# Optimization experiments

Measured on AMD Instinct MI355X. Metric: run time of the kernel, lower is better.

The kernel has to match this reference:

```python
import jax, jax.numpy as jnp
import numpy as np

D = 512
H = 8
DH = D // H
EPS = 1e-6


def _ln(x, g, b):
    m = x.mean(-1, keepdims=True)
    v = ((x - m) ** 2).mean(-1, keepdims=True)
    return g * (x - m) / jnp.sqrt(v + EPS) + b


def _mha(q_in, kv_in, W, B):
    # W: [4, D, D] = (Wq, Wk, Wv, Wo); B: [4, D]
    q = q_in @ W[0] + B[0]
    k = kv_in @ W[1] + B[1]
    v = kv_in @ W[2] + B[2]

    def split(t):
        b, l, _ = t.shape
        return t.reshape(b, l, H, DH).transpose(0, 2, 1, 3)  # [b,h,l,dh]

    q, k, v = split(q), split(k), split(v)
    s = jnp.einsum('bhqd,bhkd->bhqk', q, k) / np.sqrt(DH).astype(np.float32)
    a = jax.nn.softmax(s, axis=-1)
    o = jnp.einsum('bhqk,bhkd->bhqd', a, v)
    b_, _, l, _ = o.shape
    o = o.transpose(0, 2, 1, 3).reshape(b_, l, D)
    return o @ W[3] + B[3]


def _cross_layer(x, y, attn_w, attn_b, w1, b1, w2, b2, lns):
    # pre-norm residual sublayers (annotated-transformer style), dropout in eval mode
    x = x + _mha(_ln(x, lns[0, 0], lns[0, 1]), y, attn_w, attn_b)
    h = _ln(x, lns[1, 0], lns[1, 1])
    x = x + (jax.nn.relu(h @ w1 + b1) @ w2 + b2)
    return x


def _af(q, k, v, Wq, bq, Wo, bo):
    # AF with proj=True: single-head attention scaled by sqrt(embed_dim)
    q = q @ Wq + bq
    s = jnp.einsum('bqd,bkd->bqk', q, k) / np.sqrt(D).astype(np.float32)
    o = jax.nn.softmax(s, axis=-1) @ v
    return o @ Wo + bo


def _forward(x, text, vis,
             ft_attn_w, ft_attn_b, ft_w1, ft_b1, ft_w2, ft_b2, ft_ln,
             fv_attn_w, fv_attn_b, fv_w1, fv_b1, fv_w2, fv_b2, fv_ln,
             ldm_ln, af_w, af_b):
    # mode='y', proj=True path
    med = _cross_layer(vis, text, ft_attn_w, ft_attn_b, ft_w1, ft_b1, ft_w2, ft_b2, ft_ln)
    med = _cross_layer(med, vis, fv_attn_w, fv_attn_b, fv_w1, fv_b1, fv_w2, fv_b2, fv_ln) + med
    med = _ln(med, ldm_ln[0], ldm_ln[1])
    # FDIntervention: af_1(mediator, feature, feature) then af_2(feature, mediator, v)
    v = _af(med, x, x, af_w[0, 0], af_b[0, 0], af_w[0, 1], af_b[0, 1])
    out = _af(x, med, v, af_w[1, 0], af_b[1, 0], af_w[1, 1], af_b[1, 1])
    return out + x


def setup_inputs() -> dict:
    key = jax.random.key(0)
    ks = jax.random.split(key, 16)
    B, LX, LT, LV = 32, 256, 256, 196
    sc = 0.02

    def ln_pair():
        # [2(sublayers), 2(gamma,beta), D]
        return jnp.stack([jnp.stack([jnp.ones((D,)), jnp.zeros((D,))])] * 2)

    return {
        'x': jax.random.normal(ks[0], (B, LX, D), jnp.float32),
        'text': jax.random.normal(ks[1], (B, LT, D), jnp.float32),
        'vis': jax.random.normal(ks[2], (B, LV, D), jnp.float32),
        'ft_attn_w': jax.random.normal(ks[3], (4, D, D), jnp.float32) * sc,
        'ft_attn_b': jnp.zeros((4, D), jnp.float32),
        'ft_w1': jax.random.normal(ks[4], (D, 4 * D), jnp.float32) * sc,
        'ft_b1': jnp.zeros((4 * D,), jnp.float32),
        'ft_w2': jax.random.normal(ks[5], (4 * D, D), jnp.float32) * sc,
        'ft_b2': jnp.zeros((D,), jnp.float32),
        'ft_ln': ln_pair(),
        'fv_attn_w': jax.random.normal(ks[6], (4, D, D), jnp.float32) * sc,
        'fv_attn_b': jnp.zeros((4, D), jnp.float32),
        'fv_w1': jax.random.normal(ks[7], (D, 4 * D), jnp.float32) * sc,
        'fv_b1': jnp.zeros((4 * D,), jnp.float32),
        'fv_w2': jax.random.normal(ks[8], (4 * D, D), jnp.float32) * sc,
        'fv_b2': jnp.zeros((D,), jnp.float32),
        'fv_ln': ln_pair(),
        'ldm_ln': jnp.stack([jnp.ones((D,)), jnp.zeros((D,))]),
        'af_w': jax.random.normal(ks[9], (2, 2, D, D), jnp.float32) * sc,
        'af_b': jnp.zeros((2, 2, D), jnp.float32),
    }


def reference(x, text, vis,
              ft_attn_w, ft_attn_b, ft_w1, ft_b1, ft_w2, ft_b2, ft_ln,
              fv_attn_w, fv_attn_b, fv_w1, fv_b1, fv_w2, fv_b2, fv_ln,
              ldm_ln, af_w, af_b):
    return _forward(x, text, vis,
                    ft_attn_w, ft_attn_b, ft_w1, ft_b1, ft_w2, ft_b2, ft_ln,
                    fv_attn_w, fv_attn_b, fv_w1, fv_b1, fv_w2, fv_b2, fv_ln,
                    ldm_ln, af_w, af_b)
```

## Files before the change

### kernel.cpp

```cpp
#include <hip/hip_runtime.h>
#include <hip/hip_bf16.h>

typedef __attribute__((ext_vector_type(4))) float f32x4;
typedef __attribute__((ext_vector_type(8))) short s16x8;
typedef __attribute__((ext_vector_type(4))) short s16x4;

__device__ __forceinline__ short f2bf(float f) {
  union { float f; unsigned u; } c; c.f = f;
  unsigned r = c.u + 0x7fffu + ((c.u >> 16) & 1u);
  return (short)(r >> 16);
}
__device__ __forceinline__ float bf2f(short h) {
  union { unsigned u; float f; } c; c.u = ((unsigned)(unsigned short)h) << 16;
  return c.f;
}
__device__ __forceinline__ s16x8 cvt8(const f32x4& lo, const f32x4& hi) {
  s16x8 v;
  v[0] = f2bf(lo[0]); v[1] = f2bf(lo[1]); v[2] = f2bf(lo[2]); v[3] = f2bf(lo[3]);
  v[4] = f2bf(hi[0]); v[5] = f2bf(hi[1]); v[6] = f2bf(hi[2]); v[7] = f2bf(hi[3]);
  return v;
}

__device__ __forceinline__ void gl_lds16(const short* g, char* l) {
  __builtin_amdgcn_global_load_lds(
      (const __attribute__((address_space(1))) unsigned int*)g,
      (__attribute__((address_space(3))) unsigned int*)l, 16, 0, 0);
}

template<int CF32, int BM, int BN, int WRN, int WCN, int RING,
         int SM, int RELU, int NRES, int BIASM, int SWZ>
__global__ __launch_bounds__(WRN * WCN * 64, 2)
void gemm_k(const short* __restrict__ Ap, int hbA, long sAo, long sAi, int lda,
            const short* __restrict__ Bp, int hbB, long sBo, long sBi, int ldb,
            void* __restrict__ Cp, int hbC, long sCo, long sCi, int ldc,
            const float* __restrict__ bias,
            const float* __restrict__ res1,
            const float* __restrict__ res2,
            int M, int N, int K, float alpha, int nvalid)
{
  constexpr int WAVES = WRN * WCN;
  constexpr int T = WAVES * 64;
  constexpr int MI = BM / (WRN * 16), NI = BN / (WCN * 16);
  constexpr int ACH = BM * 8 / T, BCH = BN * 8 / T;
  constexpr int L   = ACH + BCH;
  constexpr int ABYTES = BM * 128;
  constexpr int TBYTES = (BM + BN) * 128;
  constexpr int LSTR = BN + (CF32 ? 4 : 8);
  constexpr int EPIB = BM * LSTR * (CF32 ? 4 : 2);
  constexpr int SMEMB = (RING * TBYTES > EPIB) ? RING * TBYTES : EPIB;
  __shared__ __align__(16) char smem[SMEMB];

  const int tid  = threadIdx.x;
  const int lane = tid & 63;
  const int wid  = tid >> 6;
  const int wr   = wid / WCN, wc = wid % WCN;

  int bx = blockIdx.x, by = blockIdx.y, bz = blockIdx.z;
  if constexpr (SWZ == 1) {
    const int gx = gridDim.x, gy = gridDim.y;
    const int nwg = gx * gy;
    const int o = by * gx + bx;
    const int q = nwg >> 3, r = nwg & 7;
    const int xcd = o & 7, slot = o >> 3;
    const int w = (xcd < r ? xcd * (q + 1) : r * (q + 1) + (xcd - r) * q) + slot;
    bx = w / gy; by = w - bx * gy;
  } else if constexpr (SWZ == 2) {
    const int gx = gridDim.x, gy = gridDim.y, gz = gridDim.z;
    const int nwg = gx * gy * gz;
    const int o = (bz * gy + by) * gx + bx;
    const int q = nwg >> 3, r = nwg & 7;
    const int xcd = o & 7, slot = o >> 3;
    int w = (xcd < r ? xcd * (q + 1) : r * (q + 1) + (xcd - r) * q) + slot;
    bx = w % gx; w /= gx; by = w % gy; bz = w / gy;
  }
  const int m0 = bx * BM, n0 = by * BN;
  const int z  = bz;

  const int zA = z / hbA, zAi = z - zA * hbA;
  const int zB = z / hbB, zBi = z - zB * hbB;
  const int zC = z / hbC, zCi = z - zC * hbC;
  const short* Ab = Ap + (long)zA * sAo + (long)zAi * sAi;
  const short* Bb = Bp + (long)zB * sBo + (long)zBi * sBi;
  char*        Cb = (char*)Cp + ((long)zC * sCo + (long)zCi * sCi) * (CF32 ? 4 : 2);

  int aL[ACH]; long aG[ACH];
#pragma unroll
  for (int j = 0; j < ACH; ++j) {
    int chunk = (j * WAVES + wid) * 64 + lane;
    int row = chunk >> 3;
    int c   = (chunk & 7) ^ (row & 7);
    int gr = m0 + row; if (gr > M - 1) gr = M - 1;
    aL[j] = chunk * 16;
    aG[j] = (long)gr * lda + c * 8;
  }
  int bL[BCH]; long bG[BCH];
#pragma unroll
  for (int j = 0; j < BCH; ++j) {
    int chunk = (j * WAVES + wid) * 64 + lane;
    int row = chunk >> 3;
    int c   = (chunk & 7) ^ (row & 7);
    int gc = n0 + row; if (gc > N - 1) gc = N - 1;
    bL[j] = chunk * 16;
    bG[j] = (long)gc * ldb + c * 8;
  }

  auto stage = [&](int buf, int kt) {
    const short* Akt = Ab + (long)kt * 64;
    char* base = smem + buf * TBYTES;
#pragma unroll
    for (int j = 0; j < ACH; ++j) gl_lds16(Akt + aG[j], base + aL[j]);
    const short* Bkt = Bb + (long)kt * 64;
#pragma unroll
    for (int j = 0; j < BCH; ++j) gl_lds16(Bkt + bG[j], base + ABYTES + bL[j]);
  };

  int ard[2][MI], brd[2][NI];
#pragma unroll
  for (int kk = 0; kk < 2; ++kk) {
    int kgr = kk * 4 + (lane >> 4);
#pragma unroll
    for (int mi = 0; mi < MI; ++mi) {
      int m = wr * (BM / WRN) + mi * 16 + (lane & 15);
      ard[kk][mi] = m * 128 + ((kgr ^ (m & 7)) << 4);
    }
#pragma unroll
    for (int ni = 0; ni < NI; ++ni) {
      int n = wc * (BN / WCN) + ni * 16 + (lane & 15);
      brd[kk][ni] = ABYTES + n * 128 + ((kgr ^ (n & 7)) << 4);
    }
  }

  const int NT = K >> 6;
#pragma unroll
  for (int p = 0; p < RING; ++p) if (p < NT) stage(p, p);

  f32x4 acc[MI][NI];
#pragma unroll
  for (int mi = 0; mi < MI; ++mi)
#pragma unroll
    for (int ni = 0; ni < NI; ++ni) acc[mi][ni] = (f32x4){0.f, 0.f, 0.f, 0.f};

  int bufi = 0;
  for (int t = 0; t < NT; ++t) {
    const int rem = NT - t;
    if constexpr (RING == 3) {
      if (rem >= 3)      asm volatile("s_waitcnt vmcnt(%0)" :: "n"(2 * L) : "memory");
      else if (rem == 2) asm volatile("s_waitcnt vmcnt(%0)" :: "n"(L) : "memory");
      else               asm volatile("s_waitcnt vmcnt(0)" ::: "memory");
    } else if constexpr (RING == 2) {
      if (rem >= 2)      asm volatile("s_waitcnt vmcnt(%0)" :: "n"(L) : "memory");
      else               asm volatile("s_waitcnt vmcnt(0)" ::: "memory");
    } else {
      asm volatile("s_waitcnt vmcnt(0)" ::: "memory");
    }
    asm volatile("s_barrier" ::: "memory");

    const char* base = smem + bufi * TBYTES;
#pragma unroll
    for (int kk = 0; kk < 2; ++kk) {
      s16x8 af[MI];
#pragma unroll
      for (int mi = 0; mi < MI; ++mi) af[mi] = *(const s16x8*)(base + ard[kk][mi]);
#pragma unroll
      for (int ni = 0; ni < NI; ++ni) {
        s16x8 bf = *(const s16x8*)(base + brd[kk][ni]);
#pragma unroll
        for (int mi = 0; mi < MI; ++mi)
          acc[mi][ni] = __builtin_amdgcn_mfma_f32_16x16x32_bf16(af[mi], bf, acc[mi][ni], 0, 0, 0);
      }
    }

    if (t + RING < NT) {
      asm volatile("s_waitcnt lgkmcnt(0)" ::: "memory");
      asm volatile("s_barrier" ::: "memory");
      stage(bufi, t + RING);
    }
    bufi = (bufi + 1 == RING) ? 0 : bufi + 1;
  }

  if constexpr (SM) {
#pragma unroll
    for (int mi = 0; mi < MI; ++mi) {
#pragma unroll
      for (int j = 0; j < 4; ++j) {
        float mx = -3.0e38f;
#pragma unroll
        for (int ni = 0; ni < NI; ++ni) {
          int col = n0 + wc * (BN / WCN) + ni * 16 + (lane & 15);
          float s = acc[mi][ni][j] * alpha;
          acc[mi][ni][j] = (col < nvalid) ? s : -3.0e38f;
          mx = fmaxf(mx, acc[mi][ni][j]);
        }
#pragma unroll
        for (int o = 1; o < 16; o <<= 1) mx = fmaxf(mx, __shfl_xor(mx, o));
        float sum = 0.f;
#pragma unroll
        for (int ni = 0; ni < NI; ++ni) {
          int col = n0 + wc * (BN / WCN) + ni * 16 + (lane & 15);
          float e = (col < nvalid) ? __expf(acc[mi][ni][j] - mx) : 0.f;
          acc[mi][ni][j] = e;
          sum += e;
        }
#pragma unroll
        for (int o = 1; o < 16; o <<= 1) sum += __shfl_xor(sum, o);
        float inv = 1.f / sum;
#pragma unroll
        for (int ni = 0; ni < NI; ++ni) acc[mi][ni][j] *= inv;
      }
    }
  }
  const float aep = SM ? 1.f : alpha;

  asm volatile("s_waitcnt lgkmcnt(0)" ::: "memory");
  __syncthreads();

  {
    float* lf = (float*)smem;
    short* lh = (short*)smem;
#pragma unroll
    for (int mi = 0; mi < MI; ++mi)
#pragma unroll
      for (int ni = 0; ni < NI; ++ni) {
        int c_loc = wc * (BN / WCN) + ni * 16 + (lane & 15);
        float bv = (bias && !BIASM) ? bias[n0 + c_loc] : 0.f;
        int rb = wr * (BM / WRN) + mi * 16 + ((lane >> 4) << 2);
#pragma unroll
        for (int j = 0; j < 4; ++j) {
          float v = acc[mi][ni][j] * aep + bv;
          if constexpr (CF32) lf[(rb + j) * LSTR + c_loc] = v;
          else                lh[(rb + j) * LSTR + c_loc] = f2bf(v);
        }
      }
  }
  __syncthreads();

  constexpr int CPR = BN / 8;
  constexpr int RP  = T / CPR;
  const int rr0 = tid / CPR;
  const int cc  = (tid % CPR) * 8;
  for (int r = rr0; r < BM; r += RP) {
    const int gr = m0 + r;
    if (gr >= M) break;
    f32x4 a, b;
    if constexpr (CF32) {
      a = *(const f32x4*)((const float*)smem + (long)r * LSTR + cc);
      b = *(const f32x4*)((const float*)smem + (long)r * LSTR + cc + 4);
    } else {
      s16x8 h = *(const s16x8*)((const short*)smem + (long)r * LSTR + cc);
#pragma unroll
      for (int j = 0; j < 4; ++j) { a[j] = bf2f(h[j]); b[j] = bf2f(h[j + 4]); }
    }
    if constexpr (BIASM) {
      float bm = bias[gr];
#pragma unroll
      for (int j = 0; j < 4; ++j) { a[j] += bm; b[j] += bm; }
    }
    const long gb = (long)gr * ldc + n0 + cc;
    if constexpr (NRES >= 1) {
      f32x4 r1 = *(const f32x4*)(res1 + gb), r2 = *(const f32x4*)(res1 + gb + 4);
#pragma unroll
      for (int j = 0; j < 4; ++j) { a[j] += r1[j]; b[j] += r2[j]; }
    }
    if constexpr (NRES >= 2) {
      f32x4 r1 = *(const f32x4*)(res2 + gb), r2 = *(const f32x4*)(res2 + gb + 4);
#pragma unroll
      for (int j = 0; j < 4; ++j) { a[j] += r1[j]; b[j] += r2[j]; }
    }
    if constexpr (RELU) {
#pragma unroll
      for (int j = 0; j < 4; ++j) { a[j] = fmaxf(a[j], 0.f); b[j] = fmaxf(b[j], 0.f); }
    }
    if constexpr (CF32) {
      *(f32x4*)((float*)Cb + gb) = a;
      *(f32x4*)((float*)Cb + gb + 4) = b;
    } else {
      *(s16x8*)((short*)Cb + gb) = cvt8(a, b);
    }
  }
}

__global__ __launch_bounds__(256, 2)
void mha_k(const short* __restrict__ Qp, long qStride,
           const short* __restrict__ Kp, long kStride, int ldk, int Lkv,
           const short* __restrict__ VTp, long vtStride,
           short* __restrict__ Op, int Lq, float alpha, int nvalid)
{
  __shared__ __align__(16) char smem[73728];
  char* Qs  = smem;
  char* Ks  = smem + 8192;
  char* VTs = smem + 40960;

  const int tid = threadIdx.x, lane = tid & 63, wid = tid >> 6;

  int bxr = blockIdx.x, bzr = blockIdx.z;
  {
    const int gx = gridDim.x, gz = gridDim.z;
    const int nwg = gx * gz;
    const int o = bzr * gx + bxr;
    const int q = nwg >> 3, r = nwg & 7;
    const int xcd = o & 7, slot = o >> 3;
    int w = (xcd < r ? xcd * (q + 1) : r * (q + 1) + (xcd - r) * q) + slot;
    bxr = w % gx; bzr = w / gx;
  }
  const int z = bzr, b = z >> 3, h = z & 7;
  const int m0 = bxr * 64;

  const short* Qb  = Qp + (long)b * qStride + h * 64;
  const short* Kb  = Kp + (long)b * kStride + h * 64;
  const short* VTb = VTp + (long)z * vtStride;
  short*       Ob  = Op + (long)b * qStride + h * 64;

#pragma unroll
  for (int j = 0; j < 2; ++j) {
    int chunk = (j * 4 + wid) * 64 + lane;
    int row = chunk >> 3, c = (chunk & 7) ^ (row & 7);
    int gr = m0 + row; if (gr > Lq - 1) gr = Lq - 1;
    gl_lds16(Qb + (long)gr * 512 + c * 8, Qs + chunk * 16);
  }
#pragma unroll
  for (int j = 0; j < 8; ++j) {
    int chunk = (j * 4 + wid) * 64 + lane;
    int row = chunk >> 3, c = (chunk & 7) ^ (row & 7);
    int gr = row; if (gr > Lkv - 1) gr = Lkv - 1;
    gl_lds16(Kb + (long)gr * ldk + c * 8, Ks + chunk * 16);
  }
#pragma unroll
  for (int j = 0; j < 8; ++j) {
    int chunk = (j * 4 + wid) * 64 + lane;
    int row = chunk >> 5, cw = (chunk & 31) ^ (row & 15);
    gl_lds16(VTb + (long)row * 256 + cw * 8, VTs + chunk * 16);
  }
  __syncthreads();

  f32x4 acc[16];
#pragma unroll
  for (int ni = 0; ni < 16; ++ni) acc[ni] = (f32x4){0.f, 0.f, 0.f, 0.f};
#pragma unroll
  for (int kk = 0; kk < 2; ++kk) {
    int kgr = kk * 4 + (lane >> 4);
    int m = wid * 16 + (lane & 15);
    s16x8 af = *(const s16x8*)(Qs + m * 128 + ((kgr ^ (m & 7)) << 4));
#pragma unroll
    for (int ni = 0; ni < 16; ++ni) {
      int n = ni * 16 + (lane & 15);
      s16x8 bf = *(const s16x8*)(Ks + n * 128 + ((kgr ^ (n & 7)) << 4));
      acc[ni] = __builtin_amdgcn_mfma_f32_16x16x32_bf16(af, bf, acc[ni], 0, 0, 0);
    }
  }

#pragma unroll
  for (int j = 0; j < 4; ++j) {
    float mx = -3.0e38f;
#pragma unroll
    for (int ni = 0; ni < 16; ++ni) {
      int col = ni * 16 + (lane & 15);
      float s = acc[ni][j] * alpha;
      acc[ni][j] = (col < nvalid) ? s : -3.0e38f;
      mx = fmaxf(mx, acc[ni][j]);
    }
#pragma unroll
    for (int o = 1; o < 16; o <<= 1) mx = fmaxf(mx, __shfl_xor(mx, o));
    float sum = 0.f;
#pragma unroll
    for (int ni = 0; ni < 16; ++ni) {
      int col = ni * 16 + (lane & 15);
      float e = (col < nvalid) ? __expf(acc[ni][j] - mx) : 0.f;
      acc[ni][j] = e;
      sum += e;
    }
#pragma unroll
    for (int o = 1; o < 16; o <<= 1) sum += __shfl_xor(sum, o);
    float inv = 1.f / sum;
#pragma unroll
    for (int ni = 0; ni < 16; ++ni) acc[ni][j] *= inv;
  }

  __syncthreads();

  {
    char* Ps = Ks + wid * 8192;
    const int r0 = (lane >> 4) * 4;
#pragma unroll
    for (int ni = 0; ni < 16; ++ni) {
      int col = ni * 16 + (lane & 15);
      int chunk = col >> 3, cin = (col & 7) * 2;
#pragma unroll
      for (int j = 0; j < 4; ++j) {
        int row = r0 + j;
        *(short*)(Ps + row * 512 + ((chunk ^ (row & 15)) << 4) + cin) = f2bf(acc[ni][j]);
      }
    }
  }
  asm volatile("s_waitcnt lgkmcnt(0)" ::: "memory");

  f32x4 acco[4];
#pragma unroll
  for (int ni = 0; ni < 4; ++ni) acco[ni] = (f32x4){0.f, 0.f, 0.f, 0.f};
  {
    const char* Ps = Ks + wid * 8192;
#pragma unroll
    for (int kk = 0; kk < 8; ++kk) {
      int g = lane >> 4;
      int mrow = lane & 15;
      int achunk = (kk * 4 + g) ^ (mrow & 15);
      s16x8 af = *(const s16x8*)(Ps + mrow * 512 + (achunk << 4));
#pragma unroll
      for (int ni = 0; ni < 4; ++ni) {
        int n = ni * 16 + (lane & 15);
        int bchunk = (kk * 4 + g) ^ (n & 15);
        s16x8 bf = *(const s16x8*)(VTs + n * 512 + (bchunk << 4));
        acco[ni] = __builtin_amdgcn_mfma_f32_16x16x32_bf16(af, bf, acco[ni], 0, 0, 0);
      }
    }
  }

  __syncthreads();

  {
    short* lh = (short*)smem;
#pragma unroll
    for (int ni = 0; ni < 4; ++ni) {
      int d = ni * 16 + (lane & 15);
      int rb = wid * 16 + ((lane >> 4) << 2);
#pragma unroll
      for (int j = 0; j < 4; ++j) lh[(rb + j) * 72 + d] = f2bf(acco[ni][j]);
    }
  }
  __syncthreads();
  {
    const int r0 = tid >> 3, cc = (tid & 7) * 8;
#pragma unroll
    for (int p = 0; p < 2; ++p) {
      int r = r0 + p * 32;
      int gr = m0 + r;
      if (gr < Lq) {
        s16x8 h8 = *(const s16x8*)((const short*)smem + r * 72 + cc);
        *(s16x8*)(Ob + (long)gr * 512 + cc) = h8;
      }
    }
  }
}

__global__ __launch_bounds__(256)
void prep_k(const float* ftw, const float* fvw, const float* afw,
            const float* ftw1, const float* fvw1,
            const float* ftw2, const float* fvw2,
            const float* x, const float* text,
            short* wTbase, short* dW1, short* dW2,
            short* xbf, short* textbf, short* xT)
{
  const int z = blockIdx.y, zt = blockIdx.x;

  if (z >= 16 && z < 32) {
    long off = (long)(z & 7) * 524288 + (long)zt * 2048 + threadIdx.x * 8;
    const float* src = (z < 24 ? x : text) + off;
    short* dst = (z < 24 ? xbf : textbf) + off;
    f32x4 lo = *(const f32x4*)src, hi = *(const f32x4*)(src + 4);
    *(s16x8*)dst = cvt8(lo, hi);
    return;
  }

  __shared__ float tile[64][65];
  const float* in; short* out;
  int R_in, rs_in, Rpad, tiles_r;
  if (z < 12) {
    if (zt >= 64) return;
    const int grp = z >> 2, idx = z & 3;
    in = (grp == 0 ? ftw : grp == 1 ? fvw : afw) + (long)idx * 262144;
    out = wTbase + (long)grp * 3145728 + (long)idx * 262144;
    R_in = 512; rs_in = 512; Rpad = 512; tiles_r = 8;
  } else if (z < 14) {
    const int idx = z - 12;
    in = (idx == 0 ? ftw1 : fvw1);
    out = (idx == 0 ? dW1 : dW1 + 3145728);
    R_in = 512; rs_in = 2048; Rpad = 512; tiles_r = 8;
  } else if (z < 16) {
    const int idx = z - 14;
    in = (idx == 0 ? ftw2 : fvw2);
    out = (idx == 0 ? dW2 : dW2 + 3145728);
    R_in = 2048; rs_in = 512; Rpad = 2048; tiles_r = 32;
  } else {
    if (zt >= 32) return;
    const int b = z - 32;
    in = x + (long)b * 131072;
    out = xT + (long)b * 131072;
    R_in = 256; rs_in = 512; Rpad = 256; tiles_r = 4;
  }
  const int tr = zt % tiles_r, tc = zt / tiles_r;
  const int r0 = tr * 64, c0 = tc * 64;
  const int c = threadIdx.x & 63, l0 = threadIdx.x >> 6;

#pragma unroll 4
  for (int i = 0; i < 16; ++i) {
    int l = l0 + i * 4;
    int gr = r0 + l;
    float v = 0.f;
    if (gr < R_in) v = in[(long)gr * rs_in + c0 + c];
    tile[l][c] = v;
  }
  __syncthreads();
#pragma unroll 4
  for (int i = 0; i < 16; ++i) {
    int cr = l0 + i * 4;
    out[(long)(c0 + cr) * Rpad + r0 + c] = f2bf(tile[c][cr]);
  }
}

template<int RAW>
__global__ __launch_bounds__(256)
void ln_k(const float* __restrict__ in, const float* __restrict__ g,
          const float* __restrict__ b, short* __restrict__ outp,
          short* __restrict__ rawp, int rows)
{
  int row = blockIdx.x * 4 + (threadIdx.x >> 6);
  if (row >= rows) return;
  int lane = threadIdx.x & 63;
  const float* p = in + (long)row * 512 + lane * 8;
  f32x4 v0 = *(const f32x4*)p, v1 = *(const f32x4*)(p + 4);
  if constexpr (RAW) {
    short* rp = rawp + (long)row * 512 + lane * 8;
    *(s16x8*)rp = cvt8(v0, v1);
  }
  float s = 0.f, sq = 0.f;
#pragma unroll
  for (int j = 0; j < 4; ++j) { s += v0[j] + v1[j]; sq += v0[j]*v0[j] + v1[j]*v1[j]; }
#pragma unroll
  for (int o = 1; o < 64; o <<= 1) { s += __shfl_xor(s, o); sq += __shfl_xor(sq, o); }
  float mean = s * (1.f / 512.f);
  float var  = sq * (1.f / 512.f) - mean * mean;
  float rs   = rsqrtf(var + 1e-6f);
  const f32x4 g0 = *(const f32x4*)(g + lane * 8), g1 = *(const f32x4*)(g + lane * 8 + 4);
  const f32x4 b0 = *(const f32x4*)(b + lane * 8), b1 = *(const f32x4*)(b + lane * 8 + 4);
  f32x4 o0, o1;
#pragma unroll
  for (int j = 0; j < 4; ++j) {
    o0[j] = g0[j] * (v0[j] - mean) * rs + b0[j];
    o1[j] = g1[j] * (v1[j] - mean) * rs + b1[j];
  }
  short* op = outp + (long)row * 512 + lane * 8;
  *(s16x8*)op = cvt8(o0, o1);
}

static inline int ceildiv(int a, int b) { return (a + b - 1) / b; }

template<int CF32, int BM, int BN, int WRN, int WCN, int RING,
         int SM, int RELU, int NRES, int BIASM, int SWZ>
static void launch_gemm(hipStream_t st, int gm, int gn, int gz,
                        const short* A, int hbA, long sAo, long sAi, int lda,
                        const short* B, int hbB, long sBo, long sBi, int ldb,
                        void* C, int hbC, long sCo, long sCi, int ldc,
                        const float* bias, const float* r1, const float* r2,
                        int M, int N, int K, float alpha, int nvalid)
{
  gemm_k<CF32, BM, BN, WRN, WCN, RING, SM, RELU, NRES, BIASM, SWZ>
      <<<dim3(gm, gn, gz), dim3(WRN * WCN * 64), 0, st>>>(
          A, hbA, sAo, sAi, lda, B, hbB, sBo, sBi, ldb,
          C, hbC, sCo, sCi, ldc, bias, r1, r2, M, N, K, alpha, nvalid);
}

extern "C" void kernel_launch(void* const* d_in, const int* in_sizes, int n_in,
                              void* d_out, int out_size, void* d_ws, size_t ws_size,
                              hipStream_t stream)
{
  (void)in_sizes; (void)n_in; (void)out_size; (void)ws_size;

  const float* x     = (const float*)d_in[0];
  const float* text  = (const float*)d_in[1];
  const float* vis   = (const float*)d_in[2];
  const float* ftw   = (const float*)d_in[3];
  const float* ftb   = (const float*)d_in[4];
  const float* ftw1  = (const float*)d_in[5];
  const float* ftb1  = (const float*)d_in[6];
  const float* ftw2  = (const float*)d_in[7];
  const float* ftb2  = (const float*)d_in[8];
  const float* ftln  = (const float*)d_in[9];
  const float* fvw   = (const float*)d_in[10];
  const float* fvb   = (const float*)d_in[11];
  const float* fvw1  = (const float*)d_in[12];
  const float* fvb1  = (const float*)d_in[13];
  const float* fvw2  = (const float*)d_in[14];
  const float* fvb2  = (const float*)d_in[15];
  const float* fvln  = (const float*)d_in[16];
  const float* ldmln = (const float*)d_in[17];
  const float* afw   = (const float*)d_in[18];
  const float* afb   = (const float*)d_in[19];
  float* out = (float*)d_out;

  char* ws = (char*)d_ws;
  short* wT     = (short*)ws;
  short* xbf    = (short*)(ws + 14680064);
  short* bufLN  = (short*)(ws + 23068672);
  short* bufQ   = (short*)(ws + 29491200);
  short* bufKV  = (short*)(ws + 37879808);
  short* bufT   = (short*)(ws + 54657024);
  short* bufS   = (short*)(ws + 63045632);
  short* bufO   = (short*)(ws + 88735744);
  float* bufX1  = (float*)(ws + 97124352);
  float* bufA2  = (float*)(ws + 109969408);
  short* bufMED = (short*)(ws + 122814464);
  short* bufT2  = (short*)(ws + 129236992);
  short* textbf = bufO;
  short* visbf  = (short*)bufA2;

  short* ftWq  = wT + 0;
  short* ftWk  = wT + 262144;
  short* ftWv  = wT + 524288;
  short* ftWo  = wT + 786432;
  short* ftW1t = wT + 1048576;
  short* ftW2t = wT + 2097152;
  short* fvWq  = wT + 3145728;
  short* fvWk  = wT + 3407872;
  short* fvWv  = wT + 3670016;
  short* fvWo  = wT + 3932160;
  short* fvW1t = wT + 4194304;
  short* fvW2t = wT + 5242880;
  short* afW00 = wT + 6291456;
  short* afW01 = wT + 6553600;
  short* afW10 = wT + 6815744;
  short* afW11 = wT + 7077888;

  const float AFS = 0.04419417382415922f;
  dim3 blk(256);

  prep_k<<<dim3(256, 64), blk, 0, stream>>>(
      ftw, fvw, afw, ftw1, fvw1, ftw2, fvw2, x, text,
      wT, ftW1t, ftW2t, xbf, textbf, bufT2);

  ln_k<1><<<1568, blk, 0, stream>>>(vis, ftln + 0, ftln + 512, bufLN, visbf, 6272);
  launch_gemm<0,128,64,2,2,3,0,0,0,0,1>(stream, 49,8,1, bufLN,1,0,0,512, ftWq,1,0,0,512,
      bufQ,1,0,0,512, ftb + 0, nullptr, nullptr, 6272,512,512, 1.f, 0);
  launch_gemm<0,128,64,2,2,3,0,0,0,0,1>(stream, 64,8,1, textbf,1,0,0,512, ftWk,1,0,0,512,
      bufKV,1,0,0,512, ftb + 512, nullptr, nullptr, 8192,512,512, 1.f, 0);
  launch_gemm<0,128,64,2,2,3,0,0,0,1,2>(stream, 4,4,32, ftWv,1,0,0,512, textbf,1,131072L,0L,512,
      bufT,1,131072L,0L,256, ftb + 1024, nullptr, nullptr, 512,256,512, 1.f, 0);
  mha_k<<<dim3(4,1,256), blk, 0, stream>>>(bufQ, 100352L, bufKV, 131072L, 512, 256,
      bufT, 16384L, bufO, 196, 0.125f, 256);
  launch_gemm<1,128,64,2,2,3,0,0,1,0,1>(stream, 49,8,1, bufO,1,0,0,512, ftWo,1,0,0,512,
      bufX1,1,0,0,512, ftb + 1536, vis, nullptr, 6272,512,512, 1.f, 0);
  ln_k<0><<<1568, blk, 0, stream>>>(bufX1, ftln + 1024, ftln + 1536, bufLN, nullptr, 6272);
  launch_gemm<0,128,128,2,2,2,0,1,0,0,1>(stream, 49,16,1, bufLN,1,0,0,512, ftW1t,1,0,0,512,
      bufS,1,0,0,2048, ftb1, nullptr, nullptr, 6272,2048,512, 1.f, 0);
  launch_gemm<1,128,64,2,2,3,0,0,1,0,1>(stream, 49,8,1, bufS,1,0,0,2048, ftW2t,1,0,0,2048,
      bufX1,1,0,0,512, ftb2, bufX1, nullptr, 6272,512,2048, 1.f, 0);

  ln_k<0><<<1568, blk, 0, stream>>>(bufX1, fvln + 0, fvln + 512, bufLN, nullptr, 6272);
  launch_gemm<0,128,64,2,2,3,0,0,0,0,1>(stream, 49,8,1, bufLN,1,0,0,512, fvWq,1,0,0,512,
      bufQ,1,0,0,512, fvb + 0, nullptr, nullptr, 6272,512,512, 1.f, 0);
  launch_gemm<0,128,64,2,2,3,0,0,0,0,1>(stream, 49,8,1, visbf,1,0,0,512, fvWk,1,0,0,512,
      bufKV,1,0,0,512, fvb + 512, nullptr, nullptr, 6272,512,512, 1.f, 0);
  launch_gemm<0,128,64,2,2,3,0,0,0,1,2>(stream, 4,4,32, fvWv,1,0,0,512, visbf,1,100352L,0L,512,
      bufT,1,131072L,0L,256, fvb + 1024, nullptr, nullptr, 512,196,512, 1.f, 0);
  mha_k<<<dim3(4,1,256), blk, 0, stream>>>(bufQ, 100352L, bufKV, 100352L, 512, 196,
      bufT, 16384L, bufO, 196, 0.125f, 196);
  launch_gemm<1,128,64,2,2,3,0,0,1,0,1>(stream, 49,8,1, bufO,1,0,0,512, fvWo,1,0,0,512,
      bufA2,1,0,0,512, fvb + 1536, bufX1, nullptr, 6272,512,512, 1.f, 0);
  ln_k<0><<<1568, blk, 0, stream>>>(bufA2, fvln + 1024, fvln + 1536, bufLN, nullptr, 6272);
  launch_gemm<0,128,128,2,2,2,0,1,0,0,1>(stream, 49,16,1, bufLN,1,0,0,512, fvW1t,1,0,0,512,
      bufS,1,0,0,2048, fvb1, nullptr, nullptr, 6272,2048,512, 1.f, 0);
  launch_gemm<1,128,64,2,2,3,0,0,2,0,1>(stream, 49,8,1, bufS,1,0,0,2048, fvW2t,1,0,0,2048,
      bufA2,1,0,0,512, fvb2, bufA2, bufX1, 6272,512,2048, 1.f, 0);
  ln_k<0><<<1568, blk, 0, stream>>>(bufA2, ldmln + 0, ldmln + 512, bufMED, nullptr, 6272);

  launch_gemm<0,128,64,2,2,3,0,0,0,0,1>(stream, 49,8,1, bufMED,1,0,0,512, afW00,1,0,0,512,
      bufQ,1,0,0,512, afb + 0, nullptr, nullptr, 6272,512,512, 1.f, 0);
  launch_gemm<0,32,256,2,1,2,1,0,0,0,2>(stream, 7,1,32, bufQ,1,100352L,0L,512, xbf,1,131072L,0L,512,
      bufS,1,50176L,0L,256, nullptr, nullptr, nullptr, 196,256,512, AFS, 256);
  launch_gemm<0,64,128,2,2,3,0,0,0,0,2>(stream, 4,4,32, bufS,1,50176L,0L,256, bufT2,1,131072L,0L,256,
      bufO,1,100352L,0L,512, nullptr, nullptr, nullptr, 196,512,256, 1.f, 0);
  launch_gemm<0,128,64,2,2,3,0,0,0,1,2>(stream, 4,4,32, afW01,1,0,0,512, bufO,1,100352L,0L,512,
      bufT,1,131072L,0L,256, afb + 512, nullptr, nullptr, 512,256,512, 1.f, 0);

  launch_gemm<0,128,64,2,2,3,0,0,0,0,1>(stream, 64,8,1, xbf,1,0,0,512, afW10,1,0,0,512,
      bufQ,1,0,0,512, afb + 1024, nullptr, nullptr, 8192,512,512, 1.f, 0);
  launch_gemm<0,32,256,2,1,2,1,0,0,0,2>(stream, 8,1,32, bufQ,1,131072L,0L,512, bufMED,1,100352L,0L,512,
      bufS,1,65536L,0L,256, nullptr, nullptr, nullptr, 256,256,512, AFS, 196);
  launch_gemm<0,64,128,2,2,3,0,0,0,0,2>(stream, 4,4,32, bufS,1,65536L,0L,256, bufT,1,131072L,0L,256,
      bufO,1,131072L,0L,512, nullptr, nullptr, nullptr, 256,512,256, 1.f, 0);
  launch_gemm<1,128,64,2,2,3,0,0,1,0,1>(stream, 64,8,1, bufO,1,0,0,512, afW11,1,0,0,512,
      out,1,0,0,512, afb + 1536, x, nullptr, 8192,512,512, 1.f, 0);
}
```

Measured before the change: 358.4 us.

## Merge independent GEMM pairs into single grouped launches

Adds a gemm2_k kernel that runs two independent GEMMs with the same tile configuration in one launch, splitting the grid on blockIdx.x. It is used for the Q/K projections of both cross layers, the two AF query projections, and the two AF score+softmax GEMMs. The AF schedule is reordered so the second branch's scores go to a separate buffer and are computed early. This cuts launch count and fills the GPU better with larger grids, at the cost of extra workspace, a per-block branch to pick parameters, and GEMM parameters now passed in a struct.

```diff
diff --git a/kernel.cpp b/kernel.cpp
--- a/kernel.cpp
+++ b/kernel.cpp
@@ -27,16 +27,18 @@
       (__attribute__((address_space(3))) unsigned int*)l, 16, 0, 0);
 }
 
+struct GemmP {
+  const short* A; int hbA; long sAo, sAi; int lda;
+  const short* B; int hbB; long sBo, sBi; int ldb;
+  void* C; int hbC; long sCo, sCi; int ldc;
+  const float* bias; const float* res1; const float* res2;
+  int M, N, K; float alpha; int nvalid;
+};
+
 template<int CF32, int BM, int BN, int WRN, int WCN, int RING,
-         int SM, int RELU, int NRES, int BIASM, int SWZ>
-__global__ __launch_bounds__(WRN * WCN * 64, 2)
-void gemm_k(const short* __restrict__ Ap, int hbA, long sAo, long sAi, int lda,
-            const short* __restrict__ Bp, int hbB, long sBo, long sBi, int ldb,
-            void* __restrict__ Cp, int hbC, long sCo, long sCi, int ldc,
-            const float* __restrict__ bias,
-            const float* __restrict__ res1,
-            const float* __restrict__ res2,
-            int M, int N, int K, float alpha, int nvalid)
+         int SM, int RELU, int NRES, int BIASM>
+__device__ __forceinline__
+void gemm_body(const GemmP& P, int bx, int by, int bz)
 {
   constexpr int WAVES = WRN * WCN;
   constexpr int T = WAVES * 64;
@@ -55,33 +57,15 @@
   const int wid  = tid >> 6;
   const int wr   = wid / WCN, wc = wid % WCN;
 
-  int bx = blockIdx.x, by = blockIdx.y, bz = blockIdx.z;
-  if constexpr (SWZ == 1) {
-    const int gx = gridDim.x, gy = gridDim.y;
-    const int nwg = gx * gy;
-    const int o = by * gx + bx;
-    const int q = nwg >> 3, r = nwg & 7;
-    const int xcd = o & 7, slot = o >> 3;
-    const int w = (xcd < r ? xcd * (q + 1) : r * (q + 1) + (xcd - r) * q) + slot;
-    bx = w / gy; by = w - bx * gy;
-  } else if constexpr (SWZ == 2) {
-    const int gx = gridDim.x, gy = gridDim.y, gz = gridDim.z;
-    const int nwg = gx * gy * gz;
-    const int o = (bz * gy + by) * gx + bx;
-    const int q = nwg >> 3, r = nwg & 7;
-    const int xcd = o & 7, slot = o >> 3;
-    int w = (xcd < r ? xcd * (q + 1) : r * (q + 1) + (xcd - r) * q) + slot;
-    bx = w % gx; w /= gx; by = w % gy; bz = w / gy;
-  }
   const int m0 = bx * BM, n0 = by * BN;
   const int z  = bz;
 
-  const int zA = z / hbA, zAi = z - zA * hbA;
-  const int zB = z / hbB, zBi = z - zB * hbB;
-  const int zC = z / hbC, zCi = z - zC * hbC;
-  const short* Ab = Ap + (long)zA * sAo + (long)zAi * sAi;
-  const short* Bb = Bp + (long)zB * sBo + (long)zBi * sBi;
-  char*        Cb = (char*)Cp + ((long)zC * sCo + (long)zCi * sCi) * (CF32 ? 4 : 2);
+  const int zA = z / P.hbA, zAi = z - zA * P.hbA;
+  const int zB = z / P.hbB, zBi = z - zB * P.hbB;
+  const int zC = z / P.hbC, zCi = z - zC * P.hbC;
+  const short* Ab = P.A + (long)zA * P.sAo + (long)zAi * P.sAi;
+  const short* Bb = P.B + (long)zB * P.sBo + (long)zBi * P.sBi;
+  char*        Cb = (char*)P.C + ((long)zC * P.sCo + (long)zCi * P.sCi) * (CF32 ? 4 : 2);
 
   int aL[ACH]; long aG[ACH];
 #pragma unroll
@@ -89,9 +73,9 @@
     int chunk = (j * WAVES + wid) * 64 + lane;
     int row = chunk >> 3;
     int c   = (chunk & 7) ^ (row & 7);
-    int gr = m0 + row; if (gr > M - 1) gr = M - 1;
+    int gr = m0 + row; if (gr > P.M - 1) gr = P.M - 1;
     aL[j] = chunk * 16;
-    aG[j] = (long)gr * lda + c * 8;
+    aG[j] = (long)gr * P.lda + c * 8;
   }
   int bL[BCH]; long bG[BCH];
 #pragma unroll
@@ -99,9 +83,9 @@
     int chunk = (j * WAVES + wid) * 64 + lane;
     int row = chunk >> 3;
     int c   = (chunk & 7) ^ (row & 7);
-    int gc = n0 + row; if (gc > N - 1) gc = N - 1;
+    int gc = n0 + row; if (gc > P.N - 1) gc = P.N - 1;
     bL[j] = chunk * 16;
-    bG[j] = (long)gc * ldb + c * 8;
+    bG[j] = (long)gc * P.ldb + c * 8;
   }
 
   auto stage = [&](int buf, int kt) {
@@ -130,7 +114,7 @@
     }
   }
 
-  const int NT = K >> 6;
+  const int NT = P.K >> 6;
 #pragma unroll
   for (int p = 0; p < RING; ++p) if (p < NT) stage(p, p);
 
@@ -187,8 +171,8 @@
 #pragma unroll
         for (int ni = 0; ni < NI; ++ni) {
           int col = n0 + wc * (BN / WCN) + ni * 16 + (lane & 15);
-          float s = acc[mi][ni][j] * alpha;
-          acc[mi][ni][j] = (col < nvalid) ? s : -3.0e38f;
+          float s = acc[mi][ni][j] * P.alpha;
+          acc[mi][ni][j] = (col < P.nvalid) ? s : -3.0e38f;
           mx = fmaxf(mx, acc[mi][ni][j]);
         }
 #pragma unroll
@@ -197,7 +181,7 @@
 #pragma unroll
         for (int ni = 0; ni < NI; ++ni) {
           int col = n0 + wc * (BN / WCN) + ni * 16 + (lane & 15);
-          float e = (col < nvalid) ? __expf(acc[mi][ni][j] - mx) : 0.f;
+          float e = (col < P.nvalid) ? __expf(acc[mi][ni][j] - mx) : 0.f;
           acc[mi][ni][j] = e;
           sum += e;
         }
@@ -209,7 +193,7 @@
       }
     }
   }
-  const float aep = SM ? 1.f : alpha;
+  const float aep = SM ? 1.f : P.alpha;
 
   asm volatile("s_waitcnt lgkmcnt(0)" ::: "memory");
   __syncthreads();
@@ -222,7 +206,7 @@
 #pragma unroll
       for (int ni = 0; ni < NI; ++ni) {
         int c_loc = wc * (BN / WCN) + ni * 16 + (lane & 15);
-        float bv = (bias && !BIASM) ? bias[n0 + c_loc] : 0.f;
+        float bv = (P.bias && !BIASM) ? P.bias[n0 + c_loc] : 0.f;
         int rb = wr * (BM / WRN) + mi * 16 + ((lane >> 4) << 2);
 #pragma unroll
         for (int j = 0; j < 4; ++j) {
@@ -240,7 +224,7 @@
   const int cc  = (tid % CPR) * 8;
   for (int r = rr0; r < BM; r += RP) {
     const int gr = m0 + r;
-    if (gr >= M) break;
+    if (gr >= P.M) break;
     f32x4 a, b;
     if constexpr (CF32) {
       a = *(const f32x4*)((const float*)smem + (long)r * LSTR + cc);
@@ -251,18 +235,18 @@
       for (int j = 0; j < 4; ++j) { a[j] = bf2f(h[j]); b[j] = bf2f(h[j + 4]); }
     }
     if constexpr (BIASM) {
-      float bm = bias[gr];
+      float bm = P.bias[gr];
 #pragma unroll
       for (int j = 0; j < 4; ++j) { a[j] += bm; b[j] += bm; }
     }
-    const long gb = (long)gr * ldc + n0 + cc;
+    const long gb = (long)gr * P.ldc + n0 + cc;
     if constexpr (NRES >= 1) {
-      f32x4 r1 = *(const f32x4*)(res1 + gb), r2 = *(const f32x4*)(res1 + gb + 4);
+      f32x4 r1 = *(const f32x4*)(P.res1 + gb), r2 = *(const f32x4*)(P.res1 + gb + 4);
 #pragma unroll
       for (int j = 0; j < 4; ++j) { a[j] += r1[j]; b[j] += r2[j]; }
     }
     if constexpr (NRES >= 2) {
-      f32x4 r1 = *(const f32x4*)(res2 + gb), r2 = *(const f32x4*)(res2 + gb + 4);
+      f32x4 r1 = *(const f32x4*)(P.res2 + gb), r2 = *(const f32x4*)(P.res2 + gb + 4);
 #pragma unroll
       for (int j = 0; j < 4; ++j) { a[j] += r1[j]; b[j] += r2[j]; }
     }
@@ -279,6 +263,52 @@
   }
 }
 
+__device__ __forceinline__ int xcd_remap(int o, int nwg)
+{
+  const int q = nwg >> 3, r = nwg & 7;
+  const int xcd = o & 7, slot = o >> 3;
+  return (xcd < r ? xcd * (q + 1) : r * (q + 1) + (xcd - r) * q) + slot;
+}
+
+template<int CF32, int BM, int BN, int WRN, int WCN, int RING,
+         int SM, int RELU, int NRES, int BIASM, int SWZ>
+__global__ __launch_bounds__(WRN * WCN * 64, 2)
+void gemm_k(GemmP P)
+{
+  int bx = blockIdx.x, by = blockIdx.y, bz = blockIdx.z;
+  if constexpr (SWZ == 1) {
+    const int gx = gridDim.x, gy = gridDim.y;
+    const int w = xcd_remap(by * gx + bx, gx * gy);
+    bx = w / gy; by = w - bx * gy;
+  } else if constexpr (SWZ == 2) {
+    const int gx = gridDim.x, gy = gridDim.y, gz = gridDim.z;
+    int w = xcd_remap((bz * gy + by) * gx + bx, gx * gy * gz);
+    bx = w % gx; w /= gx; by = w % gy; bz = w / gy;
+  }
+  gemm_body<CF32, BM, BN, WRN, WCN, RING, SM, RELU, NRES, BIASM>(P, bx, by, bz);
+}
+
+template<int CF32, int BM, int BN, int WRN, int WCN, int RING,
+         int SM, int RELU, int NRES, int BIASM, int SWZ>
+__global__ __launch_bounds__(WRN * WCN * 64, 2)
+void gemm2_k(GemmP p0, GemmP p1, int split)
+{
+  int bx = blockIdx.x, by = blockIdx.y, bz = blockIdx.z;
+  if constexpr (SWZ == 1) {
+    const int gx = gridDim.x, gy = gridDim.y;
+    const int w = xcd_remap(by * gx + bx, gx * gy);
+    bx = w / gy; by = w - bx * gy;
+  } else if constexpr (SWZ == 2) {
+    const int gx = gridDim.x, gy = gridDim.y, gz = gridDim.z;
+    int w = xcd_remap((bz * gy + by) * gx + bx, gx * gy * gz);
+    bx = w % gx; w /= gx; by = w % gy; bz = w / gy;
+  }
+  const bool first = (bx < split);
+  const GemmP& P = first ? p0 : p1;
+  if (!first) bx -= split;
+  gemm_body<CF32, BM, BN, WRN, WCN, RING, SM, RELU, NRES, BIASM>(P, bx, by, bz);
+}
+
 __global__ __launch_bounds__(256, 2)
 void mha_k(const short* __restrict__ Qp, long qStride,
            const short* __restrict__ Kp, long kStride, int ldk, int Lkv,
@@ -295,11 +325,7 @@
   int bxr = blockIdx.x, bzr = blockIdx.z;
   {
     const int gx = gridDim.x, gz = gridDim.z;
-    const int nwg = gx * gz;
-    const int o = bzr * gx + bxr;
-    const int q = nwg >> 3, r = nwg & 7;
-    const int xcd = o & 7, slot = o >> 3;
-    int w = (xcd < r ? xcd * (q + 1) : r * (q + 1) + (xcd - r) * q) + slot;
+    int w = xcd_remap(bzr * gx + bxr, gx * gz);
     bxr = w % gx; bzr = w / gx;
   }
   const int z = bzr, b = z >> 3, h = z & 7;
@@ -541,21 +567,19 @@
   *(s16x8*)op = cvt8(o0, o1);
 }
 
-static inline int ceildiv(int a, int b) { return (a + b - 1) / b; }
-
-template<int CF32, int BM, int BN, int WRN, int WCN, int RING,
-         int SM, int RELU, int NRES, int BIASM, int SWZ>
-static void launch_gemm(hipStream_t st, int gm, int gn, int gz,
-                        const short* A, int hbA, long sAo, long sAi, int lda,
-                        const short* B, int hbB, long sBo, long sBi, int ldb,
-                        void* C, int hbC, long sCo, long sCi, int ldc,
-                        const float* bias, const float* r1, const float* r2,
-                        int M, int N, int K, float alpha, int nvalid)
-{
-  gemm_k<CF32, BM, BN, WRN, WCN, RING, SM, RELU, NRES, BIASM, SWZ>
-      <<<dim3(gm, gn, gz), dim3(WRN * WCN * 64), 0, st>>>(
-          A, hbA, sAo, sAi, lda, B, hbB, sBo, sBi, ldb,
-          C, hbC, sCo, sCi, ldc, bias, r1, r2, M, N, K, alpha, nvalid);
+static GemmP mkP(const short* A, int hbA, long sAo, long sAi, int lda,
+                 const short* B, int hbB, long sBo, long sBi, int ldb,
+                 void* C, int hbC, long sCo, long sCi, int ldc,
+                 const float* bias, const float* r1, const float* r2,
+                 int M, int N, int K, float alpha, int nvalid)
+{
+  GemmP P;
+  P.A = A; P.hbA = hbA; P.sAo = sAo; P.sAi = sAi; P.lda = lda;
+  P.B = B; P.hbB = hbB; P.sBo = sBo; P.sBi = sBi; P.ldb = ldb;
+  P.C = C; P.hbC = hbC; P.sCo = sCo; P.sCi = sCi; P.ldc = ldc;
+  P.bias = bias; P.res1 = r1; P.res2 = r2;
+  P.M = M; P.N = N; P.K = K; P.alpha = alpha; P.nvalid = nvalid;
+  return P;
 }
 
 extern "C" void kernel_launch(void* const* d_in, const int* in_sizes, int n_in,
@@ -601,6 +625,7 @@
   short* bufT2  = (short*)(ws + 129236992);
   short* textbf = bufO;
   short* visbf  = (short*)bufA2;
+  short* bufSD  = bufS + 2097152;
 
   short* ftWq  = wT + 0;
   short* ftWk  = wT + 262144;
@@ -627,55 +652,70 @@
       wT, ftW1t, ftW2t, xbf, textbf, bufT2);
 
   ln_k<1><<<1568, blk, 0, stream>>>(vis, ftln + 0, ftln + 512, bufLN, visbf, 6272);
-  launch_gemm<0,128,64,2,2,3,0,0,0,0,1>(stream, 49,8,1, bufLN,1,0,0,512, ftWq,1,0,0,512,
-      bufQ,1,0,0,512, ftb + 0, nullptr, nullptr, 6272,512,512, 1.f, 0);
-  launch_gemm<0,128,64,2,2,3,0,0,0,0,1>(stream, 64,8,1, textbf,1,0,0,512, ftWk,1,0,0,512,
-      bufKV,1,0,0,512, ftb + 512, nullptr, nullptr, 8192,512,512, 1.f, 0);
-  launch_gemm<0,128,64,2,2,3,0,0,0,1,2>(stream, 4,4,32, ftWv,1,0,0,512, textbf,1,131072L,0L,512,
-      bufT,1,131072L,0L,256, ftb + 1024, nullptr, nullptr, 512,256,512, 1.f, 0);
+  gemm2_k<0,128,64,2,2,3,0,0,0,0,1><<<dim3(113,8,1), blk, 0, stream>>>(
+      mkP(bufLN,1,0,0,512, ftWq,1,0,0,512, bufQ,1,0,0,512,
+          ftb + 0, nullptr, nullptr, 6272,512,512, 1.f, 0),
+      mkP(textbf,1,0,0,512, ftWk,1,0,0,512, bufKV,1,0,0,512,
+          ftb + 512, nullptr, nullptr, 8192,512,512, 1.f, 0), 49);
+  gemm_k<0,128,64,2,2,3,0,0,0,1,2><<<dim3(4,4,32), blk, 0, stream>>>(
+      mkP(ftWv,1,0,0,512, textbf,1,131072L,0L,512, bufT,1,131072L,0L,256,
+          ftb + 1024, nullptr, nullptr, 512,256,512, 1.f, 0));
   mha_k<<<dim3(4,1,256), blk, 0, stream>>>(bufQ, 100352L, bufKV, 131072L, 512, 256,
       bufT, 16384L, bufO, 196, 0.125f, 256);
-  launch_gemm<1,128,64,2,2,3,0,0,1,0,1>(stream, 49,8,1, bufO,1,0,0,512, ftWo,1,0,0,512,
-      bufX1,1,0,0,512, ftb + 1536, vis, nullptr, 6272,512,512, 1.f, 0);
+  gemm_k<1,128,64,2,2,3,0,0,1,0,1><<<dim3(49,8,1), blk, 0, stream>>>(
+      mkP(bufO,1,0,0,512, ftWo,1,0,0,512, bufX1,1,0,0,512,
+          ftb + 1536, vis, nullptr, 6272,512,512, 1.f, 0));
   ln_k<0><<<1568, blk, 0, stream>>>(bufX1, ftln + 1024, ftln + 1536, bufLN, nullptr, 6272);
-  launch_gemm<0,128,128,2,2,2,0,1,0,0,1>(stream, 49,16,1, bufLN,1,0,0,512, ftW1t,1,0,0,512,
-      bufS,1,0,0,2048, ftb1, nullptr, nullptr, 6272,2048,512, 1.f, 0);
-  launch_gemm<1,128,64,2,2,3,0,0,1,0,1>(stream, 49,8,1, bufS,1,0,0,2048, ftW2t,1,0,0,2048,
-      bufX1,1,0,0,512, ftb2, bufX1, nullptr, 6272,512,2048, 1.f, 0);
+  gemm_k<0,128,128,2,2,2,0,1,0,0,1><<<dim3(49,16,1), blk, 0, stream>>>(
+      mkP(bufLN,1,0,0,512, ftW1t,1,0,0,512, bufS,1,0,0,2048,
+          ftb1, nullptr, nullptr, 6272,2048,512, 1.f, 0));
+  gemm_k<1,128,64,2,2,3,0,0,1,0,1><<<dim3(49,8,1), blk, 0, stream>>>(
+      mkP(bufS,1,0,0,2048, ftW2t,1,0,0,2048, bufX1,1,0,0,512,
+          ftb2, bufX1, nullptr, 6272,512,2048, 1.f, 0));
 
   ln_k<0><<<1568, blk, 0, stream>>>(bufX1, fvln + 0, fvln + 512, bufLN, nullptr, 6272);
-  launch_gemm<0,128,64,2,2,3,0,0,0,0,1>(stream, 49,8,1, bufLN,1,0,0,512, fvWq,1,0,0,512,
-      bufQ,1,0,0,512, fvb + 0, nullptr, nullptr, 6272,512,512, 1.f, 0);
-  launch_gemm<0,128,64,2,2,3,0,0,0,0,1>(stream, 49,8,1, visbf,1,0,0,512, fvWk,1,0,0,512,
-      bufKV,1,0,0,512, fvb + 512, nullptr, nullptr, 6272,512,512, 1.f, 0);
-  launch_gemm<0,128,64,2,2,3,0,0,0,1,2>(stream, 4,4,32, fvWv,1,0,0,512, visbf,1,100352L,0L,512,
-      bufT,1,131072L,0L,256, fvb + 1024, nullptr, nullptr, 512,196,512, 1.f, 0);
+  gemm2_k<0,128,64,2,2,3,0,0,0,0,1><<<dim3(98,8,1), blk, 0, stream>>>(
+      mkP(bufLN,1,0,0,512, fvWq,1,0,0,512, bufQ,1,0,0,512,
+          fvb + 0, nullptr, nullptr, 6272,512,512, 1.f, 0),
+      mkP(visbf,1,0,0,512, fvWk,1,0,0,512, bufKV,1,0,0,512,
+          fvb + 512, nullptr, nullptr, 6272,512,512, 1.f, 0), 49);
+  gemm_k<0,128,64,2,2,3,0,0,0,1,2><<<dim3(4,4,32), blk, 0, stream>>>(
+      mkP(fvWv,1,0,0,512, visbf,1,100352L,0L,512, bufT,1,131072L,0L,256,
+          fvb + 1024, nullptr, nullptr, 512,196,512, 1.f, 0));
   mha_k<<<dim3(4,1,256), blk, 0, stream>>>(bufQ, 100352L, bufKV, 100352L, 512, 196,
       bufT, 16384L, bufO, 196, 0.125f, 196);
-  launch_gemm<1,128,64,2,2,3,0,0,1,0,1>(stream, 49,8,1, bufO,1,0,0,512, fvWo,1,0,0,512,
-      bufA2,1,0,0,512, fvb + 1536, bufX1, nullptr, 6272,512,512, 1.f, 0);
+  gemm_k<1,128,64,2,2,3,0,0,1,0,1><<<dim3(49,8,1), blk, 0, stream>>>(
+      mkP(bufO,1,0,0,512, fvWo,1,0,0,512, bufA2,1,0,0,512,
+          fvb + 1536, bufX1, nullptr, 6272,512,512, 1.f, 0));
   ln_k<0><<<1568, blk, 0, stream>>>(bufA2, fvln + 1024, fvln + 1536, bufLN, nullptr, 6272);
-  launch_gemm<0,128,128,2,2,2,0,1,0,0,1>(stream, 49,16,1, bufLN,1,0,0,512, fvW1t,1,0,0,512,
-      bufS,1,0,0,2048, fvb1, nullptr, nullptr, 6272,2048,512, 1.f, 0);
-  launch_gemm<1,128,64,2,2,3,0,0,2,0,1>(stream, 49,8,1, bufS,1,0,0,2048, fvW2t,1,0,0,2048,
-      bufA2,1,0,0,512, fvb2, bufA2, bufX1, 6272,512,2048, 1.f, 0);
+  gemm_k<0,128,128,2,2,2,0,1,0,0,1><<<dim3(49,16,1), blk, 0, stream>>>(
+      mkP(bufLN,1,0,0,512, fvW1t,1,0,0,512, bufS,1,0,0,2048,
+          fvb1, nullptr, nullptr, 6272,2048,512, 1.f, 0));
+  gemm_k<1,128,64,2,2,3,0,0,2,0,1><<<dim3(49,8,1), blk, 0, stream>>>(
+      mkP(bufS,1,0,0,2048, fvW2t,1,0,0,2048, bufA2,1,0,0,512,
+          fvb2, bufA2, bufX1, 6272,512,2048, 1.f, 0));
   ln_k<0><<<1568, blk, 0, stream>>>(bufA2, ldmln + 0, ldmln + 512, bufMED, nullptr, 6272);
 
-  launch_gemm<0,128,64,2,2,3,0,0,0,0,1>(stream, 49,8,1, bufMED,1,0,0,512, afW00,1,0,0,512,
-      bufQ,1,0,0,512, afb + 0, nullptr, nullptr, 6272,512,512, 1.f, 0);
-  launch_gemm<0,32,256,2,1,2,1,0,0,0,2>(stream, 7,1,32, bufQ,1,100352L,0L,512, xbf,1,131072L,0L,512,
-      bufS,1,50176L,0L,256, nullptr, nullptr, nullptr, 196,256,512, AFS, 256);
-  launch_gemm<0,64,128,2,2,3,0,0,0,0,2>(stream, 4,4,32, bufS,1,50176L,0L,256, bufT2,1,131072L,0L,256,
-      bufO,1,100352L,0L,512, nullptr, nullptr, nullptr, 196,512,256, 1.f, 0);
-  launch_gemm<0,128,64,2,2,3,0,0,0,1,2>(stream, 4,4,32, afW01,1,0,0,512, bufO,1,100352L,0L,512,
-      bufT,1,131072L,0L,256, afb + 512, nullptr, nullptr, 512,256,512, 1.f, 0);
-
-  launch_gemm<0,128,64,2,2,3,0,0,0,0,1>(stream, 64,8,1, xbf,1,0,0,512, afW10,1,0,0,512,
-      bufQ,1,0,0,512, afb + 1024, nullptr, nullptr, 8192,512,512, 1.f, 0);
-  launch_gemm<0,32,256,2,1,2,1,0,0,0,2>(stream, 8,1,32, bufQ,1,131072L,0L,512, bufMED,1,100352L,0L,512,
-      bufS,1,65536L,0L,256, nullptr, nullptr, nullptr, 256,256,512, AFS, 196);
-  launch_gemm<0,64,128,2,2,3,0,0,0,0,2>(stream, 4,4,32, bufS,1,65536L,0L,256, bufT,1,131072L,0L,256,
-      bufO,1,131072L,0L,512, nullptr, nullptr, nullptr, 256,512,256, 1.f, 0);
-  launch_gemm<1,128,64,2,2,3,0,0,1,0,1>(stream, 64,8,1, bufO,1,0,0,512, afW11,1,0,0,512,
-      out,1,0,0,512, afb + 1536, x, nullptr, 8192,512,512, 1.f, 0);
-}
+  gemm2_k<0,128,64,2,2,3,0,0,0,0,1><<<dim3(113,8,1), blk, 0, stream>>>(
+      mkP(bufMED,1,0,0,512, afW00,1,0,0,512, bufQ,1,0,0,512,
+          afb + 0, nullptr, nullptr, 6272,512,512, 1.f, 0),
+      mkP(xbf,1,0,0,512, afW10,1,0,0,512, bufKV,1,0,0,512,
+          afb + 1024, nullptr, nullptr, 8192,512,512, 1.f, 0), 49);
+  gemm2_k<0,32,256,2,1,2,1,0,0,0,2><<<dim3(15,1,32), dim3(128), 0, stream>>>(
+      mkP(bufQ,1,100352L,0L,512, xbf,1,131072L,0L,512, bufS,1,50176L,0L,256,
+          nullptr, nullptr, nullptr, 196,256,512, AFS, 256),
+      mkP(bufKV,1,131072L,0L,512, bufMED,1,100352L,0L,512, bufSD,1,65536L,0L,256,
+          nullptr, nullptr, nullptr, 256,256,512, AFS, 196), 7);
+  gemm_k<0,64,128,2,2,3,0,0,0,0,2><<<dim3(4,4,32), blk, 0, stream>>>(
+      mkP(bufS,1,50176L,0L,256, bufT2,1,131072L,0L,256, bufO,1,100352L,0L,512,
+          nullptr, nullptr, nullptr, 196,512,256, 1.f, 0));
+  gemm_k<0,128,64,2,2,3,0,0,0,1,2><<<dim3(4,4,32), blk, 0, stream>>>(
+      mkP(afW01,1,0,0,512, bufO,1,100352L,0L,512, bufT,1,131072L,0L,256,
+          afb + 512, nullptr, nullptr, 512,256,512, 1.f, 0));
+  gemm_k<0,64,128,2,2,3,0,0,0,0,2><<<dim3(4,4,32), blk, 0, stream>>>(
+      mkP(bufSD,1,65536L,0L,256, bufT,1,131072L,0L,256, bufO,1,131072L,0L,512,
+          nullptr, nullptr, nullptr, 256,512,256, 1.f, 0));
+  gemm_k<1,128,64,2,2,3,0,0,1,0,1><<<dim3(64,8,1), blk, 0, stream>>>(
+      mkP(bufO,1,0,0,512, afW11,1,0,0,512, out,1,0,0,512,
+          afb + 1536, x, nullptr, 8192,512,512, 1.f, 0));
+}
```

Result: faster. 338.0 us, median of 2 (-5.7%).
